# Optimization experiments

Measured on AMD Instinct MI355X. Metric: run time of the kernel, lower is better.

The kernel has to match this reference:

```python
import jax, jax.numpy as jnp
import numpy as np

K = 3          # kernel size
STRIDE = 1
PAD = 1
DIL = 1


def setup_inputs() -> dict:
    key = jax.random.key(0)
    k1, k2, k3 = jax.random.split(key, 3)
    N, Cin, H, W = 8, 128, 64, 64
    Cout = 128
    x = jax.random.normal(k1, (N, Cin, H, W), dtype=jnp.float32)
    # offset channels: 2 * deformable_groups * K*K = 18, interleaved (dy, dx) per tap
    offset = jax.random.normal(k2, (N, 2 * K * K, H, W), dtype=jnp.float32)
    weight = jax.random.normal(k3, (Cout, Cin, K, K), dtype=jnp.float32) / np.sqrt(Cin * K * K)
    return {"x": x, "offset": offset, "weight": weight}


def _deform_conv(x, offset, weight):
    N, Cin, H, W = x.shape
    Cout = weight.shape[0]
    KK = K * K
    Ho, Wo = offset.shape[2], offset.shape[3]

    off = offset.reshape(N, KK, 2, Ho, Wo)
    dy = off[:, :, 0]  # [N, KK, Ho, Wo]
    dx = off[:, :, 1]

    kh = jnp.repeat(jnp.arange(K), K).astype(x.dtype)   # [KK]
    kw = jnp.tile(jnp.arange(K), K).astype(x.dtype)     # [KK]
    base_i = (jnp.arange(Ho) * STRIDE - PAD).astype(x.dtype)  # [Ho]
    base_j = (jnp.arange(Wo) * STRIDE - PAD).astype(x.dtype)  # [Wo]

    # Sampling positions: [N, KK, Ho, Wo]
    py = base_i[None, None, :, None] + (kh * DIL)[None, :, None, None] + dy
    px = base_j[None, None, None, :] + (kw * DIL)[None, :, None, None] + dx

    y0 = jnp.floor(py)
    x0 = jnp.floor(px)
    wy1 = py - y0
    wx1 = px - x0
    wy0 = 1.0 - wy1
    wx0 = 1.0 - wx1
    y0i = y0.astype(jnp.int32)
    x0i = x0.astype(jnp.int32)
    y1i = y0i + 1
    x1i = x0i + 1

    x_flat = x.reshape(N, Cin, H * W)

    def gather(yi, xi):
        # zero-padding outside the image
        mask = ((yi >= 0) & (yi < H) & (xi >= 0) & (xi < W)).astype(x.dtype)
        idx = jnp.clip(yi, 0, H - 1) * W + jnp.clip(xi, 0, W - 1)  # [N,KK,Ho,Wo]
        v = jnp.take_along_axis(x_flat, idx.reshape(N, 1, -1), axis=2)  # [N,Cin,KK*Ho*Wo]
        v = v.reshape(N, Cin, KK, Ho, Wo)
        return v * mask[:, None]

    sampled = (gather(y0i, x0i) * (wy0 * wx0)[:, None]
               + gather(y0i, x1i) * (wy0 * wx1)[:, None]
               + gather(y1i, x0i) * (wy1 * wx0)[:, None]
               + gather(y1i, x1i) * (wy1 * wx1)[:, None])  # [N,Cin,KK,Ho,Wo]

    w = weight.reshape(Cout, Cin, KK)
    return jnp.einsum('nckij,ock->noij', sampled, w)


def reference(x, offset, weight):
    return _deform_conv(x, offset, weight)
```

## Files before the change

kernel.cpp:

```cpp
#include <hip/hip_runtime.h>


#define H  64
#define W  64
#define CIN 128
#define COUT 128
#define NB 8
#define KK 9

typedef short bf16x8 __attribute__((ext_vector_type(8)));
typedef float f32x4  __attribute__((ext_vector_type(4)));

__device__ __forceinline__ unsigned short f2bf(float f) {
    unsigned u = __builtin_bit_cast(unsigned, f);
    u += 0x7FFFu + ((u >> 16) & 1u);
    return (unsigned short)(u >> 16);
}
__device__ __forceinline__ float lo_f(unsigned u) { return __builtin_bit_cast(float, u << 16); }
__device__ __forceinline__ float hi_f(unsigned u) { return __builtin_bit_cast(float, u & 0xFFFF0000u); }

__global__ void prep_weight(const float* __restrict__ w, unsigned short* __restrict__ wtf) {
    int id = blockIdx.x * 256 + threadIdx.x;
    int lane = id & 63;
    int ct = (id >> 6) & 3;
    int nt = (id >> 8) & 7;
    int kk = id >> 11;
    if (kk >= KK) return;
    int co = nt * 16 + (lane & 15);
    int c0 = ct * 32 + (lane >> 4) * 8;
    unsigned short v[8];
    #pragma unroll
    for (int j = 0; j < 8; ++j)
        v[j] = f2bf(w[((size_t)co * CIN + c0 + j) * KK + kk]);
    *(uint4*)(wtf + (size_t)id * 8) = *(const uint4*)v;
}

__global__ void prep_x(const float* __restrict__ x, unsigned short* __restrict__ xt) {
    __shared__ float tile[CIN][W + 1];
    int b = blockIdx.x;
    int n = b >> 6, y = b & 63;
    int t = threadIdx.x;
    int l = t & 63, g = t >> 6;
    const float* src = x + ((size_t)n * CIN * H + y) * W;
    #pragma unroll
    for (int i = 0; i < 32; ++i) {
        int c = g * 32 + i;
        tile[c][l] = src[(size_t)c * H * W + l];
    }
    __syncthreads();
    int xp = t & 63;
    int cb = (t >> 6) * 32;
    unsigned short* dst = xt + (((size_t)(n * H + y) * W + xp) * CIN + cb);
    unsigned rr[16];
    #pragma unroll
    for (int i = 0; i < 16; ++i) {
        rr[i] = (unsigned)f2bf(tile[cb + 2 * i][xp])
              | ((unsigned)f2bf(tile[cb + 2 * i + 1][xp]) << 16);
    }
    #pragma unroll
    for (int i = 0; i < 4; ++i)
        ((uint4*)dst)[i] = make_uint4(rr[4*i], rr[4*i+1], rr[4*i+2], rr[4*i+3]);
}

__global__ __launch_bounds__(256, 4) void deform_main(
        const float* __restrict__ offs, const unsigned short* __restrict__ xt,
        const unsigned short* __restrict__ wtf, float* __restrict__ out) {
    __shared__ __attribute__((aligned(16))) unsigned short samp[2][32][CIN + 8];

    int b  = blockIdx.x;
    int hh = b & 1;
    int ho = (b >> 1) & 63;
    int n  = b >> 7;
    int t = threadIdx.x;
    int lane = t & 63, wv = t >> 6;
    int lm = lane & 15, lq = lane >> 4;

    int pl = t >> 3;
    int cb = (t & 7) << 4;
    int wo_s = (hh << 5) + pl;

    const float* offp = offs + (((size_t)n * 2 * KK) * H + ho) * W + wo_s;
    const unsigned short* xbase = xt + (size_t)n * H * W * CIN + cb;

    f32x4 acc[4] = {{0,0,0,0},{0,0,0,0},{0,0,0,0},{0,0,0,0}};

    float dy = offp[0];
    float dx = offp[(size_t)H * W];
    int kh = 0, kw = 0;
    for (int kk = 0; kk < KK; ++kk) {
        float py = (float)(ho - 1 + kh) + dy;
        float px = (float)(wo_s - 1 + kw) + dx;
        float y0f = floorf(py), x0f = floorf(px);
        float wy1 = py - y0f, wx1 = px - x0f;
        float wy0 = 1.f - wy1, wx0 = 1.f - wx1;
        int y0 = (int)y0f, x0 = (int)x0f;
        int y1 = y0 + 1, x1 = x0 + 1;
        bool vy0 = (unsigned)y0 < (unsigned)H, vy1 = (unsigned)y1 < (unsigned)H;
        bool vx0 = (unsigned)x0 < (unsigned)W, vx1 = (unsigned)x1 < (unsigned)W;
        float w00 = (vy0 && vx0) ? wy0 * wx0 : 0.f;
        float w01 = (vy0 && vx1) ? wy0 * wx1 : 0.f;
        float w10 = (vy1 && vx0) ? wy1 * wx0 : 0.f;
        float w11 = (vy1 && vx1) ? wy1 * wx1 : 0.f;
        int yc0 = min(max(y0, 0), H - 1), yc1 = min(max(y1, 0), H - 1);
        int xc0 = min(max(x0, 0), W - 1), xc1 = min(max(x1, 0), W - 1);
        const unsigned short* r0 = xbase + (size_t)yc0 * (W * CIN);
        const unsigned short* r1 = xbase + (size_t)yc1 * (W * CIN);
        const unsigned short* b00 = r0 + (xc0 << 7);
        const unsigned short* b01 = r0 + (xc1 << 7);
        const unsigned short* b10 = r1 + (xc0 << 7);
        const unsigned short* b11 = r1 + (xc1 << 7);
        unsigned short* dst = &samp[kk & 1][pl][cb];
        #pragma unroll
        for (int j = 0; j < 2; ++j) {
            uint4 q00 = *(const uint4*)(b00 + 8 * j);
            uint4 q01 = *(const uint4*)(b01 + 8 * j);
            uint4 q10 = *(const uint4*)(b10 + 8 * j);
            uint4 q11 = *(const uint4*)(b11 + 8 * j);
            const unsigned* a0 = (const unsigned*)&q00;
            const unsigned* a1 = (const unsigned*)&q01;
            const unsigned* a2 = (const unsigned*)&q10;
            const unsigned* a3 = (const unsigned*)&q11;
            unsigned rr[4];
            #pragma unroll
            for (int i = 0; i < 4; ++i) {
                float v0 = w00*lo_f(a0[i]) + w01*lo_f(a1[i]) + w10*lo_f(a2[i]) + w11*lo_f(a3[i]);
                float v1 = w00*hi_f(a0[i]) + w01*hi_f(a1[i]) + w10*hi_f(a2[i]) + w11*hi_f(a3[i]);
                rr[i] = (unsigned)f2bf(v0) | ((unsigned)f2bf(v1) << 16);
            }
            *(uint4*)(dst + 8 * j) = make_uint4(rr[0], rr[1], rr[2], rr[3]);
        }
        if (kk < KK - 1) {
            dy = offp[(size_t)(2 * kk + 2) * H * W];
            dx = offp[(size_t)(2 * kk + 3) * H * W];
        }
        ++kw; if (kw == 3) { kw = 0; ++kh; }
        __syncthreads();
        const unsigned short* arow = &samp[kk & 1][((wv & 1) << 4) + lm][lq << 3];
        const unsigned short* wk = wtf + (size_t)kk * 16384
                                       + ((size_t)(wv >> 1) << 4) * 512 + (lane << 3);
        #pragma unroll
        for (int ct = 0; ct < 4; ++ct) {
            bf16x8 a = *(const bf16x8*)(arow + (ct << 5));
            #pragma unroll
            for (int i = 0; i < 4; ++i) {
                bf16x8 bf = *(const bf16x8*)(wk + ((i << 2) + ct) * 512);
                acc[i] = __builtin_amdgcn_mfma_f32_16x16x32_bf16(a, bf, acc[i], 0, 0, 0);
            }
        }
    }
    int wo = (hh << 5) + ((wv & 1) << 4) + (lq << 2);
    #pragma unroll
    for (int i = 0; i < 4; ++i) {
        int co = ((wv >> 1) << 6) + (i << 4) + lm;
        *(f32x4*)(out + (((size_t)(n * COUT + co) * H + ho) * W + wo)) = acc[i];
    }
}

extern "C" void kernel_launch(void* const* d_in, const int* in_sizes, int n_in,
                              void* d_out, int out_size, void* d_ws, size_t ws_size,
                              hipStream_t stream) {
    const float* x      = (const float*)d_in[0];
    const float* offset = (const float*)d_in[1];
    const float* weight = (const float*)d_in[2];
    float* out = (float*)d_out;

    unsigned short* xt  = (unsigned short*)d_ws;
    unsigned short* wtf = (unsigned short*)((char*)d_ws + (size_t)NB*H*W*CIN*2);

    hipLaunchKernelGGL(prep_weight, dim3(72), dim3(256), 0, stream, weight, wtf);
    hipLaunchKernelGGL(prep_x, dim3(NB * H), dim3(256), 0, stream, x, xt);
    hipLaunchKernelGGL(deform_main, dim3(NB * H * 2), dim3(256), 0, stream,
                       offset, xt, wtf, out);
}
```

Before: 112.9 us.

## Tile full output rows per block, stage weights in LDS, merge prep kernels

Each main-kernel block now covers one full output row of 64 pixels and all 128 output channels, where it previously covered 32 pixels. Per-tap weights are copied into LDS with direct global-to-LDS loads and reused across all waves, replacing per-wave global weight reads. Results are staged through LDS so the output stores are coalesced. The two prep kernels are merged into one launch. In exchange, the block count halves, LDS use grows, occupancy drops to 3 blocks, and the single sample buffer adds a second barrier per tap.

```diff
diff --git a/kernel.cpp b/kernel.cpp
--- a/kernel.cpp
+++ b/kernel.cpp
@@ -10,6 +10,8 @@
 
 typedef short bf16x8 __attribute__((ext_vector_type(8)));
 typedef float f32x4  __attribute__((ext_vector_type(4)));
+typedef __attribute__((address_space(3))) unsigned int lds_u32;
+typedef __attribute__((address_space(1))) const unsigned int gbl_u32;
 
 __device__ __forceinline__ unsigned short f2bf(float f) {
     unsigned u = __builtin_bit_cast(unsigned, f);
@@ -19,23 +21,22 @@
 __device__ __forceinline__ float lo_f(unsigned u) { return __builtin_bit_cast(float, u << 16); }
 __device__ __forceinline__ float hi_f(unsigned u) { return __builtin_bit_cast(float, u & 0xFFFF0000u); }
 
-__global__ void prep_weight(const float* __restrict__ w, unsigned short* __restrict__ wtf) {
-    int id = blockIdx.x * 256 + threadIdx.x;
-    int lane = id & 63;
-    int ct = (id >> 6) & 3;
-    int nt = (id >> 8) & 7;
-    int kk = id >> 11;
-    if (kk >= KK) return;
-    int co = nt * 16 + (lane & 15);
-    int c0 = ct * 32 + (lane >> 4) * 8;
-    unsigned short v[8];
-    #pragma unroll
-    for (int j = 0; j < 8; ++j)
-        v[j] = f2bf(w[((size_t)co * CIN + c0 + j) * KK + kk]);
-    *(uint4*)(wtf + (size_t)id * 8) = *(const uint4*)v;
-}
-
-__global__ void prep_x(const float* __restrict__ x, unsigned short* __restrict__ xt) {
+__global__ void prep_all(const float* __restrict__ x, const float* __restrict__ w,
+                         unsigned short* __restrict__ xt, unsigned short* __restrict__ wtf) {
+    if (blockIdx.x < 72) {
+        int id = blockIdx.x * 256 + threadIdx.x;
+        int lane = id & 63;
+        int ct = (id >> 6) & 3;
+        int nt = (id >> 8) & 7;
+        int kk = id >> 11;
+        int co = nt * 16 + (lane & 15);
+        int c0 = ct * 32 + (lane >> 4) * 8;
+        unsigned short v[8];
+        #pragma unroll
+        for (int j = 0; j < 8; ++j)
+            v[j] = f2bf(w[((size_t)co * CIN + c0 + j) * KK + kk]);
+        *(uint4*)(wtf + (size_t)id * 8) = *(const uint4*)v;
+    }
     __shared__ float tile[CIN][W + 1];
     int b = blockIdx.x;
     int n = b >> 6, y = b & 63;
@@ -62,34 +63,41 @@
         ((uint4*)dst)[i] = make_uint4(rr[4*i], rr[4*i+1], rr[4*i+2], rr[4*i+3]);
 }
 
-__global__ __launch_bounds__(256, 4) void deform_main(
+__global__ __launch_bounds__(256, 3) void deform_main(
         const float* __restrict__ offs, const unsigned short* __restrict__ xt,
         const unsigned short* __restrict__ wtf, float* __restrict__ out) {
-    __shared__ __attribute__((aligned(16))) unsigned short samp[2][32][CIN + 8];
+    __shared__ __attribute__((aligned(16))) char lds_raw[50176];
+    unsigned short* samp = (unsigned short*)lds_raw;
+    unsigned short* wts  = (unsigned short*)(lds_raw + 17408);
+    float* ot            = (float*)lds_raw;
 
-    int b  = blockIdx.x;
-    int hh = b & 1;
-    int ho = (b >> 1) & 63;
-    int n  = b >> 7;
+    int b = blockIdx.x;
+    int n = b >> 6, ho = b & 63;
     int t = threadIdx.x;
     int lane = t & 63, wv = t >> 6;
     int lm = lane & 15, lq = lane >> 4;
 
-    int pl = t >> 3;
-    int cb = (t & 7) << 4;
-    int wo_s = (hh << 5) + pl;
-
-    const float* offp = offs + (((size_t)n * 2 * KK) * H + ho) * W + wo_s;
+    int p  = t >> 2;
+    int cb = (t & 3) << 5;
+    const float* offp = offs + (((size_t)n * 2 * KK) * H + ho) * W + p;
     const unsigned short* xbase = xt + (size_t)n * H * W * CIN + cb;
 
-    f32x4 acc[4] = {{0,0,0,0},{0,0,0,0},{0,0,0,0},{0,0,0,0}};
+    f32x4 acc[8] = {};
 
     float dy = offp[0];
     float dx = offp[(size_t)H * W];
     int kh = 0, kw = 0;
     for (int kk = 0; kk < KK; ++kk) {
+        {
+            const unsigned short* gb = wtf + (size_t)kk * 16384 + wv * 4096;
+            unsigned short* lb = wts + wv * 4096;
+            #pragma unroll
+            for (int i = 0; i < 8; ++i)
+                __builtin_amdgcn_global_load_lds((gbl_u32*)(gb + i * 512 + lane * 8),
+                                                 (lds_u32*)(lb + i * 512), 16, 0, 0);
+        }
         float py = (float)(ho - 1 + kh) + dy;
-        float px = (float)(wo_s - 1 + kw) + dx;
+        float px = (float)(p  - 1 + kw) + dx;
         float y0f = floorf(py), x0f = floorf(px);
         float wy1 = py - y0f, wx1 = px - x0f;
         float wy0 = 1.f - wy1, wx0 = 1.f - wx1;
@@ -109,9 +117,9 @@
         const unsigned short* b01 = r0 + (xc1 << 7);
         const unsigned short* b10 = r1 + (xc0 << 7);
         const unsigned short* b11 = r1 + (xc1 << 7);
-        unsigned short* dst = &samp[kk & 1][pl][cb];
+        unsigned short* sdst = samp + p * 136 + cb;
         #pragma unroll
-        for (int j = 0; j < 2; ++j) {
+        for (int j = 0; j < 4; ++j) {
             uint4 q00 = *(const uint4*)(b00 + 8 * j);
             uint4 q01 = *(const uint4*)(b01 + 8 * j);
             uint4 q10 = *(const uint4*)(b10 + 8 * j);
@@ -127,7 +135,7 @@
                 float v1 = w00*hi_f(a0[i]) + w01*hi_f(a1[i]) + w10*hi_f(a2[i]) + w11*hi_f(a3[i]);
                 rr[i] = (unsigned)f2bf(v0) | ((unsigned)f2bf(v1) << 16);
             }
-            *(uint4*)(dst + 8 * j) = make_uint4(rr[0], rr[1], rr[2], rr[3]);
+            *(uint4*)(sdst + 8 * j) = make_uint4(rr[0], rr[1], rr[2], rr[3]);
         }
         if (kk < KK - 1) {
             dy = offp[(size_t)(2 * kk + 2) * H * W];
@@ -135,24 +143,33 @@
         }
         ++kw; if (kw == 3) { kw = 0; ++kh; }
         __syncthreads();
-        const unsigned short* arow = &samp[kk & 1][((wv & 1) << 4) + lm][lq << 3];
-        const unsigned short* wk = wtf + (size_t)kk * 16384
-                                       + ((size_t)(wv >> 1) << 4) * 512 + (lane << 3);
+        const unsigned short* arow = samp + (wv * 16 + lm) * 136 + (lq << 3);
+        const unsigned short* bbase = wts + (lane << 3);
         #pragma unroll
         for (int ct = 0; ct < 4; ++ct) {
             bf16x8 a = *(const bf16x8*)(arow + (ct << 5));
             #pragma unroll
-            for (int i = 0; i < 4; ++i) {
-                bf16x8 bf = *(const bf16x8*)(wk + ((i << 2) + ct) * 512);
-                acc[i] = __builtin_amdgcn_mfma_f32_16x16x32_bf16(a, bf, acc[i], 0, 0, 0);
+            for (int nt = 0; nt < 8; ++nt) {
+                bf16x8 bf = *(const bf16x8*)(bbase + ((nt << 2) + ct) * 512);
+                acc[nt] = __builtin_amdgcn_mfma_f32_16x16x32_bf16(a, bf, acc[nt], 0, 0, 0);
             }
         }
+        __syncthreads();
     }
-    int wo = (hh << 5) + ((wv & 1) << 4) + (lq << 2);
     #pragma unroll
-    for (int i = 0; i < 4; ++i) {
-        int co = ((wv >> 1) << 6) + (i << 4) + lm;
-        *(f32x4*)(out + (((size_t)(n * COUT + co) * H + ho) * W + wo)) = acc[i];
+    for (int nt = 0; nt < 8; ++nt) {
+        float* orow = ot + (nt * 16 + lm) * 65 + wv * 16 + (lq << 2);
+        orow[0] = acc[nt][0]; orow[1] = acc[nt][1];
+        orow[2] = acc[nt][2]; orow[3] = acc[nt][3];
+    }
+    __syncthreads();
+    int co2 = t >> 1, wo2 = (t & 1) << 5;
+    const float* srow = ot + co2 * 65 + wo2;
+    float* dstg = out + (((size_t)(n * COUT + co2) * H + ho) * W + wo2);
+    #pragma unroll
+    for (int i = 0; i < 8; ++i) {
+        f32x4 v = { srow[4*i], srow[4*i+1], srow[4*i+2], srow[4*i+3] };
+        *(f32x4*)(dstg + 4 * i) = v;
     }
 }
 
@@ -167,8 +184,7 @@
     unsigned short* xt  = (unsigned short*)d_ws;
     unsigned short* wtf = (unsigned short*)((char*)d_ws + (size_t)NB*H*W*CIN*2);
 
-    hipLaunchKernelGGL(prep_weight, dim3(72), dim3(256), 0, stream, weight, wtf);
-    hipLaunchKernelGGL(prep_x, dim3(NB * H), dim3(256), 0, stream, x, xt);
-    hipLaunchKernelGGL(deform_main, dim3(NB * H * 2), dim3(256), 0, stream,
+    hipLaunchKernelGGL(prep_all, dim3(NB * H), dim3(256), 0, stream, x, weight, xt, wtf);
+    hipLaunchKernelGGL(deform_main, dim3(NB * H), dim3(256), 0, stream,
                        offset, xt, wtf, out);
 }
```

Result: slower. 121.6 us (+7.7%).
